# Optimization experiments

Hardware: AMD Instinct MI355X
Metric: run time of the kernel (lower is better)

Reference implementation:

```python
import jax, jax.numpy as jnp
import numpy as np

N_QUBITS = 8
DEPTH = 2
DIM = 2 ** N_QUBITS

# Hadamard gate (symmetric)
_H = (1.0 / np.sqrt(2.0)) * jnp.array([[1.0, 1.0], [1.0, -1.0]], dtype=jnp.complex64)
# sign table for <Z_i>: bit of wire i is bit (n-1-i) of the basis index (wire 0 = MSB)
_bits = (np.arange(DIM)[:, None] >> np.arange(N_QUBITS - 1, -1, -1)[None, :]) & 1
_SIGNS = jnp.asarray(1.0 - 2.0 * _bits, dtype=jnp.float32)  # [DIM, n_qubits]


def _quantum(ang):
    """Vectorized statevector simulation of the circuit:
    RX(ang_i) on each wire, then DEPTH x (CNOT ladder + H on last wire);
    returns <Z_i> for each wire. ang: [R, N_QUBITS] float32 -> [R, N_QUBITS]."""
    R = ang.shape[0]
    half = ang * 0.5
    a0 = jnp.cos(half).astype(jnp.complex64)
    a1 = (jnp.sin(half) * (-1j)).astype(jnp.complex64)  # RX|0> = cos|0> - i sin|1>
    single = jnp.stack([a0, a1], axis=-1)  # [R, n, 2]
    # product state via kron over qubits (wire 0 is the most significant factor)
    state = single[:, 0]  # [R, 2]
    for q in range(1, N_QUBITS):
        state = (state[:, :, None] * single[:, q][:, None, :]).reshape(R, -1)
    for _ in range(DEPTH):
        # CNOT ladder on adjacent wires (i -> i+1)
        for i in range(N_QUBITS - 1):
            s = state.reshape(R, 2 ** i, 2, 2, -1)  # [R, pre, ctrl, tgt, post]
            s = jnp.concatenate([s[:, :, :1], s[:, :, 1:, ::-1]], axis=2)
            state = s.reshape(R, -1)
        # Hadamard on the last wire
        s = state.reshape(R, -1, 2)
        state = (s @ _H).reshape(R, -1)
    probs = state.real ** 2 + state.imag ** 2  # [R, DIM]
    return probs @ _SIGNS  # [R, n_qubits]


def setup_inputs() -> dict:
    key = jax.random.key(0)
    k_x, k_w1, k_w2 = jax.random.split(key, 3)
    B, S, E, F = 8, 4096, 1024, N_QUBITS
    x = jax.random.normal(k_x, (B, S, E), dtype=jnp.float32)
    w1 = jax.random.normal(k_w1, (F, E), dtype=jnp.float32) * 0.02
    b1 = jnp.zeros((F,), dtype=jnp.float32)
    w2 = jax.random.normal(k_w2, (E, F), dtype=jnp.float32) * 0.02
    b2 = jnp.zeros((E,), dtype=jnp.float32)
    return {"x": x, "w1": w1, "b1": b1, "w2": w2, "b2": b2}


def reference(x, w1, b1, w2, b2):
    B, S, E = x.shape
    h = jnp.einsum('bse,fe->bsf', x, w1) + b1  # linear1 -> [B, S, ffn_dim]
    q = _quantum(h.reshape(-1, N_QUBITS)).reshape(B, S, N_QUBITS)
    # dropout is identity in eval mode
    return jnp.einsum('bsf,ef->bse', q, w2) + b2  # linear2 -> [B, S, E]
```

## Files before the change

### kernel.cpp

```cpp
#include <hip/hip_runtime.h>


constexpr int THREADS = 256;
constexpr int TILE    = 16;
constexpr int E       = 1024;
constexpr int R_TOTAL = 8 * 4096;

__global__ __launch_bounds__(THREADS, 8)
void ffq_kernel(const float* __restrict__ x,
                const float* __restrict__ w1,
                const float* __restrict__ b1,
                const float* __restrict__ w2,
                const float* __restrict__ b2,
                float* __restrict__ out)
{
    __shared__ float part[TILE][33];
    __shared__ __align__(16) float qsh[TILE][8];
    __shared__ float b1s[8];

    const int t    = threadIdx.x;
    const int lane = t & 63;
    const int wid  = t >> 6;
    const int c0   = t * 4;

    if (t < 8) b1s[t] = b1[t];

    float4 w1r[8];
#pragma unroll
    for (int f = 0; f < 8; ++f)
        w1r[f] = *(const float4*)(w1 + f * E + c0);

    const int row0 = blockIdx.x * TILE;

    float4 cur = *(const float4*)(x + (size_t)row0 * E + c0);
#pragma unroll
    for (int s = 0; s < TILE; ++s) {
        const float4 xc = cur;
        if (s + 1 < TILE)
            cur = *(const float4*)(x + (size_t)(row0 + s + 1) * E + c0);

        float h[8];
#pragma unroll
        for (int f = 0; f < 8; ++f)
            h[f] = xc.x * w1r[f].x + xc.y * w1r[f].y
                 + xc.z * w1r[f].z + xc.w * w1r[f].w;

        {   const bool hb = lane & 1;
            float s0 = hb ? h[0] : h[4];
            float s1 = hb ? h[1] : h[5];
            float s2 = hb ? h[2] : h[6];
            float s3 = hb ? h[3] : h[7];
            s0 = __shfl_xor(s0, 1); s1 = __shfl_xor(s1, 1);
            s2 = __shfl_xor(s2, 1); s3 = __shfl_xor(s3, 1);
            h[0] = (hb ? h[4] : h[0]) + s0;
            h[1] = (hb ? h[5] : h[1]) + s1;
            h[2] = (hb ? h[6] : h[2]) + s2;
            h[3] = (hb ? h[7] : h[3]) + s3;
        }
        {   const bool hb = lane & 2;
            float s0 = hb ? h[0] : h[2];
            float s1 = hb ? h[1] : h[3];
            s0 = __shfl_xor(s0, 2); s1 = __shfl_xor(s1, 2);
            h[0] = (hb ? h[2] : h[0]) + s0;
            h[1] = (hb ? h[3] : h[1]) + s1;
        }
        float v;
        {   const bool hb = lane & 4;
            float s0 = hb ? h[0] : h[1];
            s0 = __shfl_xor(s0, 4);
            v = (hb ? h[1] : h[0]) + s0;
        }
        v += __shfl_xor(v, 8);
        v += __shfl_xor(v, 16);
        v += __shfl_xor(v, 32);

        if (lane < 8) {
            const int f = ((lane & 1) << 2) | (lane & 2) | ((lane >> 2) & 1);
            part[s][f * 4 + wid] = v;
        }
    }
    __syncthreads();

    if (t < TILE * 8) {
        const int r = t >> 3;
        const int f = t & 7;
        const float hq = part[r][f * 4 + 0] + part[r][f * 4 + 1]
                       + part[r][f * 4 + 2] + part[r][f * 4 + 3] + b1s[f];
        float p = __cosf(hq);
        float u = __shfl_up(p, 2, 8); if (f >= 2) p *= u;
        u = __shfl_up(p, 4, 8);       if (f >= 4) p *= u;
        const float p6 = __shfl(p, 6, 8);
        if (f == 7) p *= p6;
        qsh[r][f] = p;
    }

    float w2a[4][8];
#pragma unroll
    for (int j = 0; j < 4; ++j) {
        const float4 lo = *(const float4*)(w2 + (size_t)(c0 + j) * 8);
        const float4 hi = *(const float4*)(w2 + (size_t)(c0 + j) * 8 + 4);
        w2a[j][0] = lo.x; w2a[j][1] = lo.y; w2a[j][2] = lo.z; w2a[j][3] = lo.w;
        w2a[j][4] = hi.x; w2a[j][5] = hi.y; w2a[j][6] = hi.z; w2a[j][7] = hi.w;
    }
    const float4 b2v = *(const float4*)(b2 + c0);

    __syncthreads();

#pragma unroll
    for (int s = 0; s < TILE; ++s) {
        const float4 qlo = *(const float4*)(&qsh[s][0]);
        const float4 qhi = *(const float4*)(&qsh[s][4]);
        const float qv[8] = {qlo.x, qlo.y, qlo.z, qlo.w,
                             qhi.x, qhi.y, qhi.z, qhi.w};
        float4 o = b2v;
#pragma unroll
        for (int f = 0; f < 8; ++f) {
            o.x += qv[f] * w2a[0][f];
            o.y += qv[f] * w2a[1][f];
            o.z += qv[f] * w2a[2][f];
            o.w += qv[f] * w2a[3][f];
        }
        *(float4*)(out + (size_t)(row0 + s) * E + c0) = o;
    }
}

extern "C" void kernel_launch(void* const* d_in, const int* in_sizes, int n_in,
                              void* d_out, int out_size, void* d_ws, size_t ws_size,
                              hipStream_t stream)
{
    const float* x  = (const float*)d_in[0];
    const float* w1 = (const float*)d_in[1];
    const float* b1 = (const float*)d_in[2];
    const float* w2 = (const float*)d_in[3];
    const float* b2 = (const float*)d_in[4];
    float* out = (float*)d_out;

    ffq_kernel<<<dim3(R_TOTAL / TILE), THREADS, 0, stream>>>(x, w1, b1, w2, b2, out);
}
```

Measured before the change: 244.7 us.

## Batch four rows per iteration, double tile size, use nontemporal output stores

Each block now handles 32 rows instead of 16. The first phase loads and reduces four rows at a time, so four x loads are in flight and the four wave-shuffle reduction chains can interleave, raising memory-level and instruction-level parallelism. Output rows are written with nontemporal stores so the streamed result does not fill the cache. In exchange, register use per thread rises, the launch-bounds occupancy hint drops from 8 to 4 blocks, and there are half as many blocks.

```diff
diff --git a/kernel.cpp b/kernel.cpp
--- a/kernel.cpp
+++ b/kernel.cpp
@@ -1,12 +1,18 @@
 #include <hip/hip_runtime.h>
 
 
+typedef float f4 __attribute__((ext_vector_type(4)));
+
 constexpr int THREADS = 256;
-constexpr int TILE    = 16;
+constexpr int TILE    = 32;
+constexpr int RPI     = 4;
+constexpr int NGROUP  = TILE / RPI;
 constexpr int E       = 1024;
 constexpr int R_TOTAL = 8 * 4096;
 
-__global__ __launch_bounds__(THREADS, 8)
+static_assert(TILE * 8 == THREADS, "phase 2 uses all threads");
+
+__global__ __launch_bounds__(THREADS, 4)
 void ffq_kernel(const float* __restrict__ x,
                 const float* __restrict__ w1,
                 const float* __restrict__ b1,
@@ -25,63 +31,90 @@
 
     if (t < 8) b1s[t] = b1[t];
 
-    float4 w1r[8];
+    f4 w1r[8];
 #pragma unroll
     for (int f = 0; f < 8; ++f)
-        w1r[f] = *(const float4*)(w1 + f * E + c0);
+        w1r[f] = *(const f4*)(w1 + f * E + c0);
 
     const int row0 = blockIdx.x * TILE;
+    const float* xp = x + (size_t)row0 * E + c0;
 
-    float4 cur = *(const float4*)(x + (size_t)row0 * E + c0);
+    f4 cur[RPI];
 #pragma unroll
-    for (int s = 0; s < TILE; ++s) {
-        const float4 xc = cur;
-        if (s + 1 < TILE)
-            cur = *(const float4*)(x + (size_t)(row0 + s + 1) * E + c0);
+    for (int r = 0; r < RPI; ++r)
+        cur[r] = *(const f4*)(xp + (size_t)r * E);
 
-        float h[8];
 #pragma unroll
-        for (int f = 0; f < 8; ++f)
-            h[f] = xc.x * w1r[f].x + xc.y * w1r[f].y
-                 + xc.z * w1r[f].z + xc.w * w1r[f].w;
+    for (int g = 0; g < NGROUP; ++g) {
+        f4 xc[RPI];
+#pragma unroll
+        for (int r = 0; r < RPI; ++r) xc[r] = cur[r];
+
+        if (g + 1 < NGROUP) {
+#pragma unroll
+            for (int r = 0; r < RPI; ++r)
+                cur[r] = *(const f4*)(xp + (size_t)((g + 1) * RPI + r) * E);
+        }
+
+        float h[RPI][8];
+#pragma unroll
+        for (int r = 0; r < RPI; ++r)
+#pragma unroll
+            for (int f = 0; f < 8; ++f)
+                h[r][f] = xc[r].x * w1r[f].x + xc[r].y * w1r[f].y
+                        + xc[r].z * w1r[f].z + xc[r].w * w1r[f].w;
 
         {   const bool hb = lane & 1;
-            float s0 = hb ? h[0] : h[4];
-            float s1 = hb ? h[1] : h[5];
-            float s2 = hb ? h[2] : h[6];
-            float s3 = hb ? h[3] : h[7];
-            s0 = __shfl_xor(s0, 1); s1 = __shfl_xor(s1, 1);
-            s2 = __shfl_xor(s2, 1); s3 = __shfl_xor(s3, 1);
-            h[0] = (hb ? h[4] : h[0]) + s0;
-            h[1] = (hb ? h[5] : h[1]) + s1;
-            h[2] = (hb ? h[6] : h[2]) + s2;
-            h[3] = (hb ? h[7] : h[3]) + s3;
+#pragma unroll
+            for (int r = 0; r < RPI; ++r) {
+                float s0 = hb ? h[r][0] : h[r][4];
+                float s1 = hb ? h[r][1] : h[r][5];
+                float s2 = hb ? h[r][2] : h[r][6];
+                float s3 = hb ? h[r][3] : h[r][7];
+                s0 = __shfl_xor(s0, 1); s1 = __shfl_xor(s1, 1);
+                s2 = __shfl_xor(s2, 1); s3 = __shfl_xor(s3, 1);
+                h[r][0] = (hb ? h[r][4] : h[r][0]) + s0;
+                h[r][1] = (hb ? h[r][5] : h[r][1]) + s1;
+                h[r][2] = (hb ? h[r][6] : h[r][2]) + s2;
+                h[r][3] = (hb ? h[r][7] : h[r][3]) + s3;
+            }
         }
         {   const bool hb = lane & 2;
-            float s0 = hb ? h[0] : h[2];
-            float s1 = hb ? h[1] : h[3];
-            s0 = __shfl_xor(s0, 2); s1 = __shfl_xor(s1, 2);
-            h[0] = (hb ? h[2] : h[0]) + s0;
-            h[1] = (hb ? h[3] : h[1]) + s1;
+#pragma unroll
+            for (int r = 0; r < RPI; ++r) {
+                float s0 = hb ? h[r][0] : h[r][2];
+                float s1 = hb ? h[r][1] : h[r][3];
+                s0 = __shfl_xor(s0, 2); s1 = __shfl_xor(s1, 2);
+                h[r][0] = (hb ? h[r][2] : h[r][0]) + s0;
+                h[r][1] = (hb ? h[r][3] : h[r][1]) + s1;
+            }
         }
-        float v;
+        float v[RPI];
         {   const bool hb = lane & 4;
-            float s0 = hb ? h[0] : h[1];
-            s0 = __shfl_xor(s0, 4);
-            v = (hb ? h[1] : h[0]) + s0;
+#pragma unroll
+            for (int r = 0; r < RPI; ++r) {
+                float s0 = hb ? h[r][0] : h[r][1];
+                s0 = __shfl_xor(s0, 4);
+                v[r] = (hb ? h[r][1] : h[r][0]) + s0;
+            }
         }
-        v += __shfl_xor(v, 8);
-        v += __shfl_xor(v, 16);
-        v += __shfl_xor(v, 32);
+#pragma unroll
+        for (int r = 0; r < RPI; ++r) v[r] += __shfl_xor(v[r], 8);
+#pragma unroll
+        for (int r = 0; r < RPI; ++r) v[r] += __shfl_xor(v[r], 16);
+#pragma unroll
+        for (int r = 0; r < RPI; ++r) v[r] += __shfl_xor(v[r], 32);
 
         if (lane < 8) {
             const int f = ((lane & 1) << 2) | (lane & 2) | ((lane >> 2) & 1);
-            part[s][f * 4 + wid] = v;
+#pragma unroll
+            for (int r = 0; r < RPI; ++r)
+                part[g * RPI + r][f * 4 + wid] = v[r];
         }
     }
     __syncthreads();
 
-    if (t < TILE * 8) {
+    {
         const int r = t >> 3;
         const int f = t & 7;
         const float hq = part[r][f * 4 + 0] + part[r][f * 4 + 1]
@@ -97,22 +130,22 @@
     float w2a[4][8];
 #pragma unroll
     for (int j = 0; j < 4; ++j) {
-        const float4 lo = *(const float4*)(w2 + (size_t)(c0 + j) * 8);
-        const float4 hi = *(const float4*)(w2 + (size_t)(c0 + j) * 8 + 4);
+        const f4 lo = *(const f4*)(w2 + (size_t)(c0 + j) * 8);
+        const f4 hi = *(const f4*)(w2 + (size_t)(c0 + j) * 8 + 4);
         w2a[j][0] = lo.x; w2a[j][1] = lo.y; w2a[j][2] = lo.z; w2a[j][3] = lo.w;
         w2a[j][4] = hi.x; w2a[j][5] = hi.y; w2a[j][6] = hi.z; w2a[j][7] = hi.w;
     }
-    const float4 b2v = *(const float4*)(b2 + c0);
+    const f4 b2v = *(const f4*)(b2 + c0);
 
     __syncthreads();
 
 #pragma unroll
     for (int s = 0; s < TILE; ++s) {
-        const float4 qlo = *(const float4*)(&qsh[s][0]);
-        const float4 qhi = *(const float4*)(&qsh[s][4]);
+        const f4 qlo = *(const f4*)(&qsh[s][0]);
+        const f4 qhi = *(const f4*)(&qsh[s][4]);
         const float qv[8] = {qlo.x, qlo.y, qlo.z, qlo.w,
                              qhi.x, qhi.y, qhi.z, qhi.w};
-        float4 o = b2v;
+        f4 o = b2v;
 #pragma unroll
         for (int f = 0; f < 8; ++f) {
             o.x += qv[f] * w2a[0][f];
@@ -120,7 +153,7 @@
             o.z += qv[f] * w2a[2][f];
             o.w += qv[f] * w2a[3][f];
         }
-        *(float4*)(out + (size_t)(row0 + s) * E + c0) = o;
+        __builtin_nontemporal_store(o, (f4*)(out + (size_t)(row0 + s) * E + c0));
     }
 }
 
```

Result: no change. 241.8 us (-1.2%).

## Use single-wave blocks that each own whole rows, removing cross-wave reduction

Applied to the files above, without the earlier changes.

Each 64-thread block now handles 16 full rows. Every lane keeps four column chunks of w1 and w2 in registers, so the per-row reduction finishes with wave shuffles and needs no shared-memory partial sums or extra barrier. Output stores become nontemporal to avoid polluting cache. The cost is much higher register pressure (128 floats of w2 plus 128 of w1) and fewer, smaller blocks, which may lower occupancy and the memory-level parallelism available to a bandwidth-bound kernel.

```diff
diff --git a/kernel.cpp b/kernel.cpp
--- a/kernel.cpp
+++ b/kernel.cpp
@@ -1,12 +1,14 @@
 #include <hip/hip_runtime.h>
 
 
-constexpr int THREADS = 256;
-constexpr int TILE    = 16;
+typedef float f4 __attribute__((ext_vector_type(4)));
+
+constexpr int THREADS = 64;
+constexpr int PW      = 16;
 constexpr int E       = 1024;
 constexpr int R_TOTAL = 8 * 4096;
 
-__global__ __launch_bounds__(THREADS, 8)
+__global__ __launch_bounds__(THREADS, 2)
 void ffq_kernel(const float* __restrict__ x,
                 const float* __restrict__ w1,
                 const float* __restrict__ b1,
@@ -14,58 +16,76 @@
                 const float* __restrict__ b2,
                 float* __restrict__ out)
 {
-    __shared__ float part[TILE][33];
-    __shared__ __align__(16) float qsh[TILE][8];
-    __shared__ float b1s[8];
+    __shared__ __align__(16) float qsh[PW][8];
 
-    const int t    = threadIdx.x;
-    const int lane = t & 63;
-    const int wid  = t >> 6;
-    const int c0   = t * 4;
+    const int L    = threadIdx.x;
+    const int f    = L & 7;
+    const int row0 = blockIdx.x * PW;
 
-    if (t < 8) b1s[t] = b1[t];
+    f4 w1r[8][4];
+#pragma unroll
+    for (int ff = 0; ff < 8; ++ff)
+#pragma unroll
+        for (int k = 0; k < 4; ++k)
+            w1r[ff][k] = *(const f4*)(w1 + ff * E + k * 256 + L * 4);
 
-    float4 w1r[8];
+    const float b1v = b1[f];
+
+    const float* xp = x + (size_t)row0 * E + L * 4;
+
+    f4 cur[4];
 #pragma unroll
-    for (int f = 0; f < 8; ++f)
-        w1r[f] = *(const float4*)(w1 + f * E + c0);
+    for (int k = 0; k < 4; ++k)
+        cur[k] = *(const f4*)(xp + k * 256);
 
-    const int row0 = blockIdx.x * TILE;
+#pragma unroll
+    for (int r = 0; r < PW; ++r) {
+        f4 xc[4];
+#pragma unroll
+        for (int k = 0; k < 4; ++k) xc[k] = cur[k];
 
-    float4 cur = *(const float4*)(x + (size_t)row0 * E + c0);
+        if (r + 1 < PW) {
 #pragma unroll
-    for (int s = 0; s < TILE; ++s) {
-        const float4 xc = cur;
-        if (s + 1 < TILE)
-            cur = *(const float4*)(x + (size_t)(row0 + s + 1) * E + c0);
+            for (int k = 0; k < 4; ++k)
+                cur[k] = *(const f4*)(xp + (size_t)(r + 1) * E + k * 256);
+        }
 
         float h[8];
 #pragma unroll
-        for (int f = 0; f < 8; ++f)
-            h[f] = xc.x * w1r[f].x + xc.y * w1r[f].y
-                 + xc.z * w1r[f].z + xc.w * w1r[f].w;
+        for (int ff = 0; ff < 8; ++ff) {
+            float s;
+            s  = xc[0].x * w1r[ff][0].x + xc[0].y * w1r[ff][0].y
+               + xc[0].z * w1r[ff][0].z + xc[0].w * w1r[ff][0].w;
+            s += xc[1].x * w1r[ff][1].x + xc[1].y * w1r[ff][1].y
+               + xc[1].z * w1r[ff][1].z + xc[1].w * w1r[ff][1].w;
+            s += xc[2].x * w1r[ff][2].x + xc[2].y * w1r[ff][2].y
+               + xc[2].z * w1r[ff][2].z + xc[2].w * w1r[ff][2].w;
+            s += xc[3].x * w1r[ff][3].x + xc[3].y * w1r[ff][3].y
+               + xc[3].z * w1r[ff][3].z + xc[3].w * w1r[ff][3].w;
+            h[ff] = s;
+        }
 
-        {   const bool hb = lane & 1;
-            float s0 = hb ? h[0] : h[4];
-            float s1 = hb ? h[1] : h[5];
-            float s2 = hb ? h[2] : h[6];
-            float s3 = hb ? h[3] : h[7];
+        {   const bool hb = L & 1;
+            float s0 = hb ? h[0] : h[1];
+            float s1 = hb ? h[2] : h[3];
+            float s2 = hb ? h[4] : h[5];
+            float s3 = hb ? h[6] : h[7];
             s0 = __shfl_xor(s0, 1); s1 = __shfl_xor(s1, 1);
             s2 = __shfl_xor(s2, 1); s3 = __shfl_xor(s3, 1);
-            h[0] = (hb ? h[4] : h[0]) + s0;
-            h[1] = (hb ? h[5] : h[1]) + s1;
-            h[2] = (hb ? h[6] : h[2]) + s2;
-            h[3] = (hb ? h[7] : h[3]) + s3;
+            h[0] = (hb ? h[1] : h[0]) + s0;
+            h[1] = (hb ? h[3] : h[2]) + s1;
+            h[2] = (hb ? h[5] : h[4]) + s2;
+            h[3] = (hb ? h[7] : h[6]) + s3;
         }
-        {   const bool hb = lane & 2;
-            float s0 = hb ? h[0] : h[2];
-            float s1 = hb ? h[1] : h[3];
+        {   const bool hb = L & 2;
+            float s0 = hb ? h[0] : h[1];
+            float s1 = hb ? h[2] : h[3];
             s0 = __shfl_xor(s0, 2); s1 = __shfl_xor(s1, 2);
-            h[0] = (hb ? h[2] : h[0]) + s0;
-            h[1] = (hb ? h[3] : h[1]) + s1;
+            h[0] = (hb ? h[1] : h[0]) + s0;
+            h[1] = (hb ? h[3] : h[2]) + s1;
         }
         float v;
-        {   const bool hb = lane & 4;
+        {   const bool hb = L & 4;
             float s0 = hb ? h[0] : h[1];
             s0 = __shfl_xor(s0, 4);
             v = (hb ? h[1] : h[0]) + s0;
@@ -74,53 +94,53 @@
         v += __shfl_xor(v, 16);
         v += __shfl_xor(v, 32);
 
-        if (lane < 8) {
-            const int f = ((lane & 1) << 2) | (lane & 2) | ((lane >> 2) & 1);
-            part[s][f * 4 + wid] = v;
-        }
-    }
-    __syncthreads();
-
-    if (t < TILE * 8) {
-        const int r = t >> 3;
-        const int f = t & 7;
-        const float hq = part[r][f * 4 + 0] + part[r][f * 4 + 1]
-                       + part[r][f * 4 + 2] + part[r][f * 4 + 3] + b1s[f];
-        float p = __cosf(hq);
+        float p = __cosf(v + b1v);
         float u = __shfl_up(p, 2, 8); if (f >= 2) p *= u;
         u = __shfl_up(p, 4, 8);       if (f >= 4) p *= u;
         const float p6 = __shfl(p, 6, 8);
         if (f == 7) p *= p6;
-        qsh[r][f] = p;
+
+        if (L < 8) qsh[r][L] = p;
     }
-
-    float w2a[4][8];
-#pragma unroll
-    for (int j = 0; j < 4; ++j) {
-        const float4 lo = *(const float4*)(w2 + (size_t)(c0 + j) * 8);
-        const float4 hi = *(const float4*)(w2 + (size_t)(c0 + j) * 8 + 4);
-        w2a[j][0] = lo.x; w2a[j][1] = lo.y; w2a[j][2] = lo.z; w2a[j][3] = lo.w;
-        w2a[j][4] = hi.x; w2a[j][5] = hi.y; w2a[j][6] = hi.z; w2a[j][7] = hi.w;
-    }
-    const float4 b2v = *(const float4*)(b2 + c0);
 
     __syncthreads();
 
+    float w2a[4][4][8];
 #pragma unroll
-    for (int s = 0; s < TILE; ++s) {
-        const float4 qlo = *(const float4*)(&qsh[s][0]);
-        const float4 qhi = *(const float4*)(&qsh[s][4]);
+    for (int k = 0; k < 4; ++k)
+#pragma unroll
+        for (int j = 0; j < 4; ++j) {
+            const f4 lo = *(const f4*)(w2 + (size_t)(k * 256 + L * 4 + j) * 8);
+            const f4 hi = *(const f4*)(w2 + (size_t)(k * 256 + L * 4 + j) * 8 + 4);
+            w2a[k][j][0] = lo.x; w2a[k][j][1] = lo.y;
+            w2a[k][j][2] = lo.z; w2a[k][j][3] = lo.w;
+            w2a[k][j][4] = hi.x; w2a[k][j][5] = hi.y;
+            w2a[k][j][6] = hi.z; w2a[k][j][7] = hi.w;
+        }
+    f4 b2r[4];
+#pragma unroll
+    for (int k = 0; k < 4; ++k)
+        b2r[k] = *(const f4*)(b2 + k * 256 + L * 4);
+
+#pragma unroll
+    for (int r = 0; r < PW; ++r) {
+        const f4 qlo = *(const f4*)(&qsh[r][0]);
+        const f4 qhi = *(const f4*)(&qsh[r][4]);
         const float qv[8] = {qlo.x, qlo.y, qlo.z, qlo.w,
                              qhi.x, qhi.y, qhi.z, qhi.w};
-        float4 o = b2v;
 #pragma unroll
-        for (int f = 0; f < 8; ++f) {
-            o.x += qv[f] * w2a[0][f];
-            o.y += qv[f] * w2a[1][f];
-            o.z += qv[f] * w2a[2][f];
-            o.w += qv[f] * w2a[3][f];
+        for (int k = 0; k < 4; ++k) {
+            f4 o = b2r[k];
+#pragma unroll
+            for (int ff = 0; ff < 8; ++ff) {
+                o.x += qv[ff] * w2a[k][0][ff];
+                o.y += qv[ff] * w2a[k][1][ff];
+                o.z += qv[ff] * w2a[k][2][ff];
+                o.w += qv[ff] * w2a[k][3][ff];
+            }
+            __builtin_nontemporal_store(
+                o, (f4*)(out + (size_t)(row0 + r) * E + k * 256 + L * 4));
         }
-        *(float4*)(out + (size_t)(row0 + s) * E + c0) = o;
     }
 }
 
@@ -135,5 +155,5 @@
     const float* b2 = (const float*)d_in[4];
     float* out = (float*)d_out;
 
-    ffq_kernel<<<dim3(R_TOTAL / TILE), THREADS, 0, stream>>>(x, w1, b1, w2, b2, out);
+    ffq_kernel<<<dim3(R_TOTAL / PW), THREADS, 0, stream>>>(x, w1, b1, w2, b2, out);
 }
```

Result: no change. 244.1 us (-0.3%).

## Replace cross-lane shuffles with DPP row reductions and deepen x prefetch

Applied to the files above, without the earlier changes.

The in-wave reduction of the eight projection values now uses DPP quad permutes and row shifts instead of ds_bpermute-based shuffles. It stops at 16-lane row granularity and writes partial sums into a larger padded shared buffer, which the reduction thread then sums over 16 entries. It also prefetches two rows of x ahead instead of one and writes the output with nontemporal stores. The aim is to cut LDS-permute latency and instruction count in the reduction and to keep more loads in flight. In exchange it uses more shared memory and adds extra serial adds in the final reduction.

```diff
diff --git a/kernel.cpp b/kernel.cpp
--- a/kernel.cpp
+++ b/kernel.cpp
@@ -1,10 +1,18 @@
 #include <hip/hip_runtime.h>
 
+
+typedef float f4 __attribute__((ext_vector_type(4)));
 
 constexpr int THREADS = 256;
 constexpr int TILE    = 16;
 constexpr int E       = 1024;
 constexpr int R_TOTAL = 8 * 4096;
+
+template<int CTRL>
+__device__ __forceinline__ float dppf(float v) {
+    return __int_as_float(__builtin_amdgcn_update_dpp(
+        0, __float_as_int(v), CTRL, 0xF, 0xF, true));
+}
 
 __global__ __launch_bounds__(THREADS, 8)
 void ffq_kernel(const float* __restrict__ x,
@@ -14,7 +22,7 @@
                 const float* __restrict__ b2,
                 float* __restrict__ out)
 {
-    __shared__ float part[TILE][33];
+    __shared__ float part[TILE * 16 * 9];
     __shared__ __align__(16) float qsh[TILE][8];
     __shared__ float b1s[8];
 
@@ -25,19 +33,27 @@
 
     if (t < 8) b1s[t] = b1[t];
 
-    float4 w1r[8];
+    f4 w1r[8];
 #pragma unroll
     for (int f = 0; f < 8; ++f)
-        w1r[f] = *(const float4*)(w1 + f * E + c0);
+        w1r[f] = *(const f4*)(w1 + f * E + c0);
 
     const int row0 = blockIdx.x * TILE;
+    const float* xp = x + (size_t)row0 * E + c0;
 
-    float4 cur = *(const float4*)(x + (size_t)row0 * E + c0);
+    const bool writer = (lane & 12) == 0;
+    const int  jj     = wid * 4 + (lane >> 4);
+    const int  fb     = lane & 3;
+
+    f4 cur0 = *(const f4*)(xp);
+    f4 cur1 = *(const f4*)(xp + E);
+
 #pragma unroll
     for (int s = 0; s < TILE; ++s) {
-        const float4 xc = cur;
-        if (s + 1 < TILE)
-            cur = *(const float4*)(x + (size_t)(row0 + s + 1) * E + c0);
+        const f4 xc = cur0;
+        cur0 = cur1;
+        if (s + 2 < TILE)
+            cur1 = *(const f4*)(xp + (size_t)(s + 2) * E);
 
         float h[8];
 #pragma unroll
@@ -45,38 +61,35 @@
             h[f] = xc.x * w1r[f].x + xc.y * w1r[f].y
                  + xc.z * w1r[f].z + xc.w * w1r[f].w;
 
-        {   const bool hb = lane & 1;
-            float s0 = hb ? h[0] : h[4];
-            float s1 = hb ? h[1] : h[5];
-            float s2 = hb ? h[2] : h[6];
-            float s3 = hb ? h[3] : h[7];
-            s0 = __shfl_xor(s0, 1); s1 = __shfl_xor(s1, 1);
-            s2 = __shfl_xor(s2, 1); s3 = __shfl_xor(s3, 1);
-            h[0] = (hb ? h[4] : h[0]) + s0;
-            h[1] = (hb ? h[5] : h[1]) + s1;
-            h[2] = (hb ? h[6] : h[2]) + s2;
-            h[3] = (hb ? h[7] : h[3]) + s3;
+        {
+            const bool hb = lane & 1;
+            float s0 = hb ? h[0] : h[1];
+            float s1 = hb ? h[2] : h[3];
+            float s2 = hb ? h[4] : h[5];
+            float s3 = hb ? h[6] : h[7];
+            s0 = dppf<0xB1>(s0); s1 = dppf<0xB1>(s1);
+            s2 = dppf<0xB1>(s2); s3 = dppf<0xB1>(s3);
+            h[0] = (hb ? h[1] : h[0]) + s0;
+            h[1] = (hb ? h[3] : h[2]) + s1;
+            h[2] = (hb ? h[5] : h[4]) + s2;
+            h[3] = (hb ? h[7] : h[6]) + s3;
         }
-        {   const bool hb = lane & 2;
-            float s0 = hb ? h[0] : h[2];
-            float s1 = hb ? h[1] : h[3];
-            s0 = __shfl_xor(s0, 2); s1 = __shfl_xor(s1, 2);
-            h[0] = (hb ? h[2] : h[0]) + s0;
-            h[1] = (hb ? h[3] : h[1]) + s1;
+        float v0, v1;
+        {
+            const bool hb = lane & 2;
+            float s0 = hb ? h[0] : h[1];
+            float s1 = hb ? h[2] : h[3];
+            s0 = dppf<0x4E>(s0); s1 = dppf<0x4E>(s1);
+            v0 = (hb ? h[1] : h[0]) + s0;
+            v1 = (hb ? h[3] : h[2]) + s1;
         }
-        float v;
-        {   const bool hb = lane & 4;
-            float s0 = hb ? h[0] : h[1];
-            s0 = __shfl_xor(s0, 4);
-            v = (hb ? h[1] : h[0]) + s0;
-        }
-        v += __shfl_xor(v, 8);
-        v += __shfl_xor(v, 16);
-        v += __shfl_xor(v, 32);
+        v0 += dppf<0x124>(v0);  v1 += dppf<0x124>(v1);
+        v0 += dppf<0x128>(v0);  v1 += dppf<0x128>(v1);
 
-        if (lane < 8) {
-            const int f = ((lane & 1) << 2) | (lane & 2) | ((lane >> 2) & 1);
-            part[s][f * 4 + wid] = v;
+        if (writer) {
+            const int w = (s * 16 + jj) * 9 + fb;
+            part[w]     = v0;
+            part[w + 4] = v1;
         }
     }
     __syncthreads();
@@ -84,8 +97,10 @@
     if (t < TILE * 8) {
         const int r = t >> 3;
         const int f = t & 7;
-        const float hq = part[r][f * 4 + 0] + part[r][f * 4 + 1]
-                       + part[r][f * 4 + 2] + part[r][f * 4 + 3] + b1s[f];
+        float hq = b1s[f];
+#pragma unroll
+        for (int j = 0; j < 16; ++j)
+            hq += part[(r * 16 + j) * 9 + f];
         float p = __cosf(hq);
         float u = __shfl_up(p, 2, 8); if (f >= 2) p *= u;
         u = __shfl_up(p, 4, 8);       if (f >= 4) p *= u;
@@ -97,22 +112,22 @@
     float w2a[4][8];
 #pragma unroll
     for (int j = 0; j < 4; ++j) {
-        const float4 lo = *(const float4*)(w2 + (size_t)(c0 + j) * 8);
-        const float4 hi = *(const float4*)(w2 + (size_t)(c0 + j) * 8 + 4);
+        const f4 lo = *(const f4*)(w2 + (size_t)(c0 + j) * 8);
+        const f4 hi = *(const f4*)(w2 + (size_t)(c0 + j) * 8 + 4);
         w2a[j][0] = lo.x; w2a[j][1] = lo.y; w2a[j][2] = lo.z; w2a[j][3] = lo.w;
         w2a[j][4] = hi.x; w2a[j][5] = hi.y; w2a[j][6] = hi.z; w2a[j][7] = hi.w;
     }
-    const float4 b2v = *(const float4*)(b2 + c0);
+    const f4 b2v = *(const f4*)(b2 + c0);
 
     __syncthreads();
 
 #pragma unroll
     for (int s = 0; s < TILE; ++s) {
-        const float4 qlo = *(const float4*)(&qsh[s][0]);
-        const float4 qhi = *(const float4*)(&qsh[s][4]);
+        const f4 qlo = *(const f4*)(&qsh[s][0]);
+        const f4 qhi = *(const f4*)(&qsh[s][4]);
         const float qv[8] = {qlo.x, qlo.y, qlo.z, qlo.w,
                              qhi.x, qhi.y, qhi.z, qhi.w};
-        float4 o = b2v;
+        f4 o = b2v;
 #pragma unroll
         for (int f = 0; f < 8; ++f) {
             o.x += qv[f] * w2a[0][f];
@@ -120,7 +135,7 @@
             o.z += qv[f] * w2a[2][f];
             o.w += qv[f] * w2a[3][f];
         }
-        *(float4*)(out + (size_t)(row0 + s) * E + c0) = o;
+        __builtin_nontemporal_store(o, (f4*)(out + (size_t)(row0 + s) * E + c0));
     }
 }
 
```

After: 242.2 us. No clear change (-1.0%).
